# Kernel optimization log

Hardware: AMD Instinct MI355X
Metric: run time of the kernel (lower is better)

Reference implementation:

```python
import jax, jax.numpy as jnp
import numpy as np

MARGIN = 0.3
EPS = 1e-12


def setup_inputs() -> dict:
    key = jax.random.key(0)
    k1, k2, k3 = jax.random.split(key, 3)
    B, D = 8192, 1024
    features = jax.random.normal(k1, (B, D), dtype=jnp.float32)
    labels = jax.random.randint(k2, (B,), 0, 100, dtype=jnp.int64)
    domain_labels = jax.random.randint(k3, (B,), 0, 2, dtype=jnp.int64)
    return {"features": features, "labels": labels, "domain_labels": domain_labels}


def reference(features, labels, domain_labels):
    # L2-normalize rows (F.normalize: x / max(||x||, eps))
    norm = jnp.maximum(jnp.linalg.norm(features, axis=1, keepdims=True), EPS)
    f = features / norm

    herb = domain_labels == 0   # [B] anchors
    field = domain_labels == 1  # [B] candidates

    sq = jnp.sum(f * f, axis=1)                                   # [B]
    d2 = sq[:, None] + sq[None, :] - 2.0 * jnp.einsum('id,jd->ij', f, f)
    d = jnp.sqrt(jnp.maximum(d2, 0.0))                            # [B, B]

    same = labels[:, None] == labels[None, :]                     # [B, B]
    pair = herb[:, None] & field[None, :]
    pos_mask = pair & same
    neg_mask = pair & ~same

    INF = jnp.float32(jnp.inf)
    pos_min = jnp.min(jnp.where(pos_mask, d, INF), axis=1)        # [B]
    neg_min = jnp.min(jnp.where(neg_mask, d, INF), axis=1)        # [B]

    valid = herb & jnp.any(pos_mask, axis=1) & jnp.any(neg_mask, axis=1)
    # Substitute 0 for invalid rows BEFORE subtracting to avoid inf - inf.
    pos_s = jnp.where(valid, pos_min, 0.0)
    neg_s = jnp.where(valid, neg_min, 0.0)
    tl = jnp.maximum(pos_s - neg_s + MARGIN, 0.0)                 # [B]

    loss_sum = jnp.sum(jnp.where(valid, tl, 0.0))
    count = jnp.sum(valid.astype(jnp.float32))
    return jnp.where(count > 0, loss_sum / jnp.maximum(count, 1.0), 0.0)
```

## Files before the change

kernel.cpp:

```cpp
#include <hip/hip_runtime.h>


#define B_ROWS 8192
#define DIM    1024

typedef __bf16 bf16x8 __attribute__((ext_vector_type(8)));
typedef float  f32x4  __attribute__((ext_vector_type(4)));

__device__ __forceinline__ unsigned short f2bf_rne(float x) {
    unsigned u = __float_as_uint(x);
    unsigned r = (u + 0x7FFFu + ((u >> 16) & 1u)) >> 16;
    return (unsigned short)r;
}
__device__ __forceinline__ float bf2f(unsigned short h) {
    return __uint_as_float(((unsigned)h) << 16);
}

__device__ __forceinline__ void async_copy16(const void* g, void* l) {
    __builtin_amdgcn_global_load_lds(
        (const __attribute__((address_space(1))) unsigned int*)g,
        (__attribute__((address_space(3))) unsigned int*)l,
        16, 0, 0);
}

__global__ __launch_bounds__(256) void compute_slots(
    const int* __restrict__ dom, int* __restrict__ slotOf,
    unsigned* __restrict__ cnt)
{
    __shared__ int cnts[256];
    __shared__ int base[257];
    const int t = threadIdx.x;
    const int p0 = t * 32;

    unsigned mask = 0u; int c = 0;
    #pragma unroll
    for (int i = 0; i < 32; ++i) {
        const int isA = (dom[p0 + i] == 0) ? 1 : 0;
        mask |= ((unsigned)isA) << i;
        c += isA;
    }
    cnts[t] = c;
    __syncthreads();
    if (t == 0) {
        int acc = 0;
        for (int i = 0; i < 256; ++i) { base[i] = acc; acc += cnts[i]; }
        base[256] = acc;
        cnt[0] = (unsigned)acc;
    }
    __syncthreads();
    const int nA = base[256];
    int aB = base[t];
    #pragma unroll
    for (int i = 0; i < 32; ++i) {
        const int isA = (mask >> i) & 1;
        slotOf[p0 + i] = isA ? aB : nA + (p0 + i - aB);
        aB += isA;
    }
}

__global__ __launch_bounds__(256) void normalize_rows(
    const float* __restrict__ feat, const int* __restrict__ labels,
    const int* __restrict__ slotOf, unsigned short* __restrict__ G,
    int* __restrict__ labG, float* __restrict__ sqG)
{
    const int wv = threadIdx.x >> 6, lane = threadIdx.x & 63;
    const int row = blockIdx.x * 4 + wv;

    const float4* src = (const float4*)(feat + (size_t)row * DIM);
    float4 v[4];
    float ss = 0.0f;
    #pragma unroll
    for (int j = 0; j < 4; ++j) {
        v[j] = src[j * 64 + lane];
        ss += v[j].x * v[j].x + v[j].y * v[j].y + v[j].z * v[j].z + v[j].w * v[j].w;
    }
    #pragma unroll
    for (int s = 32; s > 0; s >>= 1) ss += __shfl_xor(ss, s);
    const float inv = 1.0f / fmaxf(sqrtf(ss), 1e-12f);

    const int slot = slotOf[row];
    unsigned short ub[16];
    float ss2 = 0.0f;
    #pragma unroll
    for (int j = 0; j < 4; ++j) {
        const float f0 = v[j].x * inv, f1 = v[j].y * inv,
                    f2 = v[j].z * inv, f3 = v[j].w * inv;
        ub[j * 4 + 0] = f2bf_rne(f0); ub[j * 4 + 1] = f2bf_rne(f1);
        ub[j * 4 + 2] = f2bf_rne(f2); ub[j * 4 + 3] = f2bf_rne(f3);
        #pragma unroll
        for (int q = 0; q < 4; ++q) {
            const float fr = bf2f(ub[j * 4 + q]);
            ss2 += fr * fr;
        }
    }
    #pragma unroll
    for (int s = 32; s > 0; s >>= 1) ss2 += __shfl_xor(ss2, s);
    if (lane == 0) {
        sqG[slot]  = ss2;
        labG[slot] = labels[row];
    }
    ushort4* dst = (ushort4*)(G + (size_t)slot * DIM);
    #pragma unroll
    for (int j = 0; j < 4; ++j) {
        ushort4 pk;
        pk.x = ub[j * 4 + 0]; pk.y = ub[j * 4 + 1];
        pk.z = ub[j * 4 + 2]; pk.w = ub[j * 4 + 3];
        dst[j * 64 + lane] = pk;
    }
}

__global__ __launch_bounds__(256) void tile_mindist(
    const unsigned short* __restrict__ G, const int* __restrict__ labG,
    const float* __restrict__ sqG, const unsigned* __restrict__ cnt,
    unsigned* __restrict__ posmin, unsigned* __restrict__ negmin)
{
    const int nA = (int)cnt[0];
    const int nF = B_ROWS - nA;
    const int nTA = (nA + 127) >> 7;
    const int nTF = (nF + 127) >> 7;
    const int total = nTA * nTF;

    __shared__ __align__(16) unsigned short S[2][2][128 * 32];

    const int t = threadIdx.x;
    const int lane = t & 63, w = t >> 6;
    const int wm = w >> 1, wn = w & 1;
    const int l15 = lane & 15, quad = lane >> 4;

    const int ch0 = 2 * w;
    const int crow = lane >> 2;
    const int cbyte = (lane & 3) * 16;

    const int rdA = (wm * 64 + l15) * 32 + quad * 8;
    const int rdF = (wn * 64 + l15) * 32 + quad * 8;

    const char* Gb = (const char*)G;

    for (int tile = blockIdx.x; tile < total; tile += gridDim.x) {
        const int tx = tile % nTA;
        const int ty = tile / nTA;
        const int rowA0 = tx * 128;
        const int rowF0 = nA + ty * 128;

        const char* ga[2]; const char* gf[2];
        #pragma unroll
        for (int h = 0; h < 2; ++h) {
            const int ch = ch0 + h;
            const int rA = rowA0 + 16 * ch + crow;
            int rF = rowF0 + 16 * ch + crow;
            if (rF > B_ROWS - 1) rF = B_ROWS - 1;
            ga[h] = Gb + (size_t)rA * (DIM * 2) + cbyte;
            gf[h] = Gb + (size_t)rF * (DIM * 2) + cbyte;
        }

        f32x4 acc[4][4] = {};

        #pragma unroll
        for (int h = 0; h < 2; ++h) {
            async_copy16(ga[h], &S[0][0][(ch0 + h) * 512]);
            async_copy16(gf[h], &S[0][1][(ch0 + h) * 512]);
        }
        __syncthreads();

        #pragma unroll 4
        for (int step = 0; step < 32; ++step) {
            const int cur = step & 1;
            const int nb = cur ^ 1;
            if (step < 31) {
                const int off = (step + 1) * 64;
                #pragma unroll
                for (int h = 0; h < 2; ++h) {
                    async_copy16(ga[h] + off, &S[nb][0][(ch0 + h) * 512]);
                    async_copy16(gf[h] + off, &S[nb][1][(ch0 + h) * 512]);
                }
            }

            const unsigned short* pa = &S[cur][0][rdA];
            const unsigned short* pf = &S[cur][1][rdF];
            bf16x8 a[4], b[4];
            #pragma unroll
            for (int fm = 0; fm < 4; ++fm) a[fm] = *(const bf16x8*)(pa + fm * 512);
            #pragma unroll
            for (int fn = 0; fn < 4; ++fn) b[fn] = *(const bf16x8*)(pf + fn * 512);
            #pragma unroll
            for (int fm = 0; fm < 4; ++fm)
                #pragma unroll
                for (int fn = 0; fn < 4; ++fn)
                    acc[fm][fn] = __builtin_amdgcn_mfma_f32_16x16x32_bf16(
                        a[fm], b[fn], acc[fm][fn], 0, 0, 0);

            __syncthreads();
        }

        const float INFV = __uint_as_float(0x7f800000u);
        float sqf[4]; int lf_[4]; bool vf[4];
        #pragma unroll
        for (int fn = 0; fn < 4; ++fn) {
            const int rf = rowF0 + wn * 64 + fn * 16 + l15;
            vf[fn] = rf < B_ROWS;
            const int rc = vf[fn] ? rf : (B_ROWS - 1);
            sqf[fn] = sqG[rc];
            lf_[fn] = labG[rc];
        }
        #pragma unroll
        for (int fm = 0; fm < 4; ++fm) {
            #pragma unroll
            for (int r = 0; r < 4; ++r) {
                const int ra = rowA0 + wm * 64 + fm * 16 + quad * 4 + r;
                const bool va = ra < nA;
                const int rac = va ? ra : 0;
                const float sqa = sqG[rac];
                const int la_ = labG[rac];
                float pmin = INFV, nmin = INFV;
                #pragma unroll
                for (int fn = 0; fn < 4; ++fn) {
                    const float dd = fmaxf(sqa + sqf[fn] - 2.0f * acc[fm][fn][r], 0.0f);
                    if (vf[fn]) {
                        if (la_ == lf_[fn]) pmin = fminf(pmin, dd);
                        else                nmin = fminf(nmin, dd);
                    }
                }
                #pragma unroll
                for (int s = 1; s < 16; s <<= 1) {
                    pmin = fminf(pmin, __shfl_xor(pmin, s));
                    nmin = fminf(nmin, __shfl_xor(nmin, s));
                }
                if (l15 == 0 && va) {
                    if (pmin < INFV) atomicMin(&posmin[ra], __float_as_uint(pmin));
                    if (nmin < INFV) atomicMin(&negmin[ra], __float_as_uint(nmin));
                }
            }
        }
        __syncthreads();
    }
}

__global__ __launch_bounds__(256) void reduce_loss(
    const unsigned* __restrict__ posmin, const unsigned* __restrict__ negmin,
    float* __restrict__ accum)
{
    const int i = blockIdx.x * 256 + threadIdx.x;
    const unsigned up = posmin[i], un = negmin[i];
    float tl = 0.0f, c = 0.0f;
    if (up != 0xFFFFFFFFu && un != 0xFFFFFFFFu) {
        const float pd = sqrtf(__uint_as_float(up));
        const float nd = sqrtf(__uint_as_float(un));
        tl = fmaxf(pd - nd + 0.3f, 0.0f);
        c = 1.0f;
    }
    #pragma unroll
    for (int s = 32; s > 0; s >>= 1) {
        tl += __shfl_down(tl, s);
        c  += __shfl_down(c, s);
    }
    __shared__ float sb[8];
    const int lane = threadIdx.x & 63, w = threadIdx.x >> 6;
    if (lane == 0) { sb[w] = tl; sb[4 + w] = c; }
    __syncthreads();
    if (threadIdx.x == 0) {
        atomicAdd(&accum[0], sb[0] + sb[1] + sb[2] + sb[3]);
        atomicAdd(&accum[1], sb[4] + sb[5] + sb[6] + sb[7]);
    }
}

__global__ void finalize(const float* __restrict__ accum, float* __restrict__ out) {
    const float s = accum[0], c = accum[1];
    out[0] = (c > 0.0f) ? s / fmaxf(c, 1.0f) : 0.0f;
}

extern "C" void kernel_launch(void* const* d_in, const int* in_sizes, int n_in,
                              void* d_out, int out_size, void* d_ws, size_t ws_size,
                              hipStream_t stream) {
    const float* feat  = (const float*)d_in[0];
    const int* labels  = (const int*)d_in[1];
    const int* dom     = (const int*)d_in[2];
    float* out = (float*)d_out;

    char* ws = (char*)d_ws;
    unsigned short* G   = (unsigned short*)(ws);
    int*      labG      = (int*)(ws + 16777216);
    float*    sqG       = (float*)(ws + 16809984);
    unsigned* posmin    = (unsigned*)(ws + 16842752);
    unsigned* negmin    = (unsigned*)(ws + 16875520);
    unsigned* cnt       = (unsigned*)(ws + 16908288);
    float*    accum     = (float*)(ws + 16908296);
    int*      slotOf    = (int*)(ws + 16842752);

    hipMemsetAsync(cnt, 0, 16, stream);

    compute_slots<<<1, 256, 0, stream>>>(dom, slotOf, cnt);
    normalize_rows<<<B_ROWS / 4, 256, 0, stream>>>(feat, labels, slotOf,
                                                   G, labG, sqG);

    hipMemsetAsync(posmin, 0xFF, 65536, stream);

    tile_mindist<<<1056, 256, 0, stream>>>(G, labG, sqG, cnt, posmin, negmin);

    reduce_loss<<<B_ROWS / 256, 256, 0, stream>>>(posmin, negmin, accum);
    finalize<<<1, 1, 0, stream>>>(accum, out);
}
```

Measured before the change: 180.5 us.

## Single-buffer K=64 LDS tiles in mindist GEMM and fuse loss reduction kernels

The tile GEMM's double-buffered 32-wide K slices are replaced by single-buffered 64-wide slices, so the main loop runs 16 steps with two MFMA K-substeps each. The idea is to halve loop iterations and barrier-paired steps. The cost is that the next slice's global loads now start only after compute finishes, so they no longer overlap the MFMAs. Separately, the multi-block reduce, its finalize kernel and the accumulator memset are replaced by one single-block kernel that writes the output directly. This removes launches and atomics but also drops the memset that zeroed the row counter.

After: 244.0 us. 1.35x slower.

```diff
diff --git a/kernel.cpp b/kernel.cpp
--- a/kernel.cpp
+++ b/kernel.cpp
@@ -120,19 +120,20 @@
     const int nTF = (nF + 127) >> 7;
     const int total = nTA * nTF;
 
-    __shared__ __align__(16) unsigned short S[2][2][128 * 32];
+    __shared__ __align__(16) unsigned short As[128 * 64];
+    __shared__ __align__(16) unsigned short Fs[128 * 64];
 
     const int t = threadIdx.x;
     const int lane = t & 63, w = t >> 6;
     const int wm = w >> 1, wn = w & 1;
     const int l15 = lane & 15, quad = lane >> 4;
 
-    const int ch0 = 2 * w;
-    const int crow = lane >> 2;
-    const int cbyte = (lane & 3) * 16;
-
-    const int rdA = (wm * 64 + l15) * 32 + quad * 8;
-    const int rdF = (wn * 64 + l15) * 32 + quad * 8;
+    const int c0 = 4 * w;
+    const int crow = lane >> 3;
+    const int cbyte = (lane & 7) * 16;
+
+    const int rdA = (wm * 64 + l15) * 64 + quad * 8;
+    const int rdF = (wn * 64 + l15) * 64 + quad * 8;
 
     const char* Gb = (const char*)G;
 
@@ -142,12 +143,12 @@
         const int rowA0 = tx * 128;
         const int rowF0 = nA + ty * 128;
 
-        const char* ga[2]; const char* gf[2];
-        #pragma unroll
-        for (int h = 0; h < 2; ++h) {
-            const int ch = ch0 + h;
-            const int rA = rowA0 + 16 * ch + crow;
-            int rF = rowF0 + 16 * ch + crow;
+        const char* ga[4]; const char* gf[4];
+        #pragma unroll
+        for (int h = 0; h < 4; ++h) {
+            const int c = c0 + h;
+            const int rA = rowA0 + 8 * c + crow;
+            int rF = rowF0 + 8 * c + crow;
             if (rF > B_ROWS - 1) rF = B_ROWS - 1;
             ga[h] = Gb + (size_t)rA * (DIM * 2) + cbyte;
             gf[h] = Gb + (size_t)rF * (DIM * 2) + cbyte;
@@ -156,40 +157,42 @@
         f32x4 acc[4][4] = {};
 
         #pragma unroll
-        for (int h = 0; h < 2; ++h) {
-            async_copy16(ga[h], &S[0][0][(ch0 + h) * 512]);
-            async_copy16(gf[h], &S[0][1][(ch0 + h) * 512]);
-        }
-        __syncthreads();
-
-        #pragma unroll 4
-        for (int step = 0; step < 32; ++step) {
-            const int cur = step & 1;
-            const int nb = cur ^ 1;
-            if (step < 31) {
-                const int off = (step + 1) * 64;
-                #pragma unroll
-                for (int h = 0; h < 2; ++h) {
-                    async_copy16(ga[h] + off, &S[nb][0][(ch0 + h) * 512]);
-                    async_copy16(gf[h] + off, &S[nb][1][(ch0 + h) * 512]);
+        for (int h = 0; h < 4; ++h) {
+            async_copy16(ga[h], &As[(c0 + h) * 512]);
+            async_copy16(gf[h], &Fs[(c0 + h) * 512]);
+        }
+
+        for (int step = 0; step < 16; ++step) {
+            __syncthreads();
+
+            bf16x8 a[4][2], b[4][2];
+            #pragma unroll
+            for (int u = 0; u < 2; ++u) {
+                #pragma unroll
+                for (int fm = 0; fm < 4; ++fm)
+                    a[fm][u] = *(const bf16x8*)(&As[rdA + fm * 1024 + u * 32]);
+                #pragma unroll
+                for (int fn = 0; fn < 4; ++fn)
+                    b[fn][u] = *(const bf16x8*)(&Fs[rdF + fn * 1024 + u * 32]);
+            }
+            #pragma unroll
+            for (int u = 0; u < 2; ++u)
+                #pragma unroll
+                for (int fm = 0; fm < 4; ++fm)
+                    #pragma unroll
+                    for (int fn = 0; fn < 4; ++fn)
+                        acc[fm][fn] = __builtin_amdgcn_mfma_f32_16x16x32_bf16(
+                            a[fm][u], b[fn][u], acc[fm][fn], 0, 0, 0);
+
+            __syncthreads();
+            if (step < 15) {
+                const int off = (step + 1) * 128;
+                #pragma unroll
+                for (int h = 0; h < 4; ++h) {
+                    async_copy16(ga[h] + off, &As[(c0 + h) * 512]);
+                    async_copy16(gf[h] + off, &Fs[(c0 + h) * 512]);
                 }
             }
-
-            const unsigned short* pa = &S[cur][0][rdA];
-            const unsigned short* pf = &S[cur][1][rdF];
-            bf16x8 a[4], b[4];
-            #pragma unroll
-            for (int fm = 0; fm < 4; ++fm) a[fm] = *(const bf16x8*)(pa + fm * 512);
-            #pragma unroll
-            for (int fn = 0; fn < 4; ++fn) b[fn] = *(const bf16x8*)(pf + fn * 512);
-            #pragma unroll
-            for (int fm = 0; fm < 4; ++fm)
-                #pragma unroll
-                for (int fn = 0; fn < 4; ++fn)
-                    acc[fm][fn] = __builtin_amdgcn_mfma_f32_16x16x32_bf16(
-                        a[fm], b[fn], acc[fm][fn], 0, 0, 0);
-
-            __syncthreads();
         }
 
         const float INFV = __uint_as_float(0x7f800000u);
@@ -235,18 +238,23 @@
     }
 }
 
-__global__ __launch_bounds__(256) void reduce_loss(
+__global__ __launch_bounds__(256) void reduce_one(
     const unsigned* __restrict__ posmin, const unsigned* __restrict__ negmin,
-    float* __restrict__ accum)
+    float* __restrict__ out)
 {
-    const int i = blockIdx.x * 256 + threadIdx.x;
-    const unsigned up = posmin[i], un = negmin[i];
+    const int t = threadIdx.x;
+    const int lane = t & 63, w = t >> 6;
     float tl = 0.0f, c = 0.0f;
-    if (up != 0xFFFFFFFFu && un != 0xFFFFFFFFu) {
-        const float pd = sqrtf(__uint_as_float(up));
-        const float nd = sqrtf(__uint_as_float(un));
-        tl = fmaxf(pd - nd + 0.3f, 0.0f);
-        c = 1.0f;
+    #pragma unroll
+    for (int j = 0; j < 32; ++j) {
+        const int i = j * 256 + t;
+        const unsigned up = posmin[i], un = negmin[i];
+        if (up != 0xFFFFFFFFu && un != 0xFFFFFFFFu) {
+            const float pd = sqrtf(__uint_as_float(up));
+            const float nd = sqrtf(__uint_as_float(un));
+            tl += fmaxf(pd - nd + 0.3f, 0.0f);
+            c += 1.0f;
+        }
     }
     #pragma unroll
     for (int s = 32; s > 0; s >>= 1) {
@@ -254,18 +262,13 @@
         c  += __shfl_down(c, s);
     }
     __shared__ float sb[8];
-    const int lane = threadIdx.x & 63, w = threadIdx.x >> 6;
     if (lane == 0) { sb[w] = tl; sb[4 + w] = c; }
     __syncthreads();
-    if (threadIdx.x == 0) {
-        atomicAdd(&accum[0], sb[0] + sb[1] + sb[2] + sb[3]);
-        atomicAdd(&accum[1], sb[4] + sb[5] + sb[6] + sb[7]);
-    }
-}
-
-__global__ void finalize(const float* __restrict__ accum, float* __restrict__ out) {
-    const float s = accum[0], c = accum[1];
-    out[0] = (c > 0.0f) ? s / fmaxf(c, 1.0f) : 0.0f;
+    if (t == 0) {
+        const float s = sb[0] + sb[1] + sb[2] + sb[3];
+        const float cc = sb[4] + sb[5] + sb[6] + sb[7];
+        out[0] = (cc > 0.0f) ? s / fmaxf(cc, 1.0f) : 0.0f;
+    }
 }
 
 extern "C" void kernel_launch(void* const* d_in, const int* in_sizes, int n_in,
@@ -283,10 +286,7 @@
     unsigned* posmin    = (unsigned*)(ws + 16842752);
     unsigned* negmin    = (unsigned*)(ws + 16875520);
     unsigned* cnt       = (unsigned*)(ws + 16908288);
-    float*    accum     = (float*)(ws + 16908296);
     int*      slotOf    = (int*)(ws + 16842752);
-
-    hipMemsetAsync(cnt, 0, 16, stream);
 
     compute_slots<<<1, 256, 0, stream>>>(dom, slotOf, cnt);
     normalize_rows<<<B_ROWS / 4, 256, 0, stream>>>(feat, labels, slotOf,
@@ -296,6 +296,5 @@
 
     tile_mindist<<<1056, 256, 0, stream>>>(G, labG, sqG, cnt, posmin, negmin);
 
-    reduce_loss<<<B_ROWS / 256, 256, 0, stream>>>(posmin, negmin, accum);
-    finalize<<<1, 1, 0, stream>>>(accum, out);
-}
+    reduce_one<<<1, 256, 0, stream>>>(posmin, negmin, out);
+}
```

## Map tile strips to XCDs for L2 reuse and fuse loss reduction kernels

Applied to the files above, without the earlier changes.

Tiles are now assigned so that the blocks landing on each XCD (blockIdx & 7) share a contiguous strip of candidate tiles, which keeps those candidate rows resident in that XCD's L2 instead of spreading tiles across all caches. The separate reduce and finalize kernels, the accumulator and one memset are replaced by a single-block kernel that reduces all 8192 rows and writes the output directly. This removes launch and atomic overhead. In exchange the final reduction runs on one block only, and correctness now relies on compute_slots initialising cnt without the removed memset.

New measurement: 182.9 us. Within noise of the previous version (+1.3%).

```diff
diff --git a/kernel.cpp b/kernel.cpp
--- a/kernel.cpp
+++ b/kernel.cpp
@@ -118,7 +118,13 @@
     const int nF = B_ROWS - nA;
     const int nTA = (nA + 127) >> 7;
     const int nTF = (nF + 127) >> 7;
-    const int total = nTA * nTF;
+    if (nTA == 0 || nTF == 0) return;
+
+    const int strip = (nTF + 7) >> 3;
+    const int xcd  = blockIdx.x & 7;
+    const int slot = blockIdx.x >> 3;
+    const int tyBase = xcd * strip;
+    const int nloc = nTA * strip;
 
     __shared__ __align__(16) unsigned short S[2][2][128 * 32];
 
@@ -136,9 +142,10 @@
 
     const char* Gb = (const char*)G;
 
-    for (int tile = blockIdx.x; tile < total; tile += gridDim.x) {
-        const int tx = tile % nTA;
-        const int ty = tile / nTA;
+    for (int idx = slot; idx < nloc; idx += 132) {
+        const int ty = tyBase + idx / nTA;
+        if (ty >= nTF) break;
+        const int tx = idx % nTA;
         const int rowA0 = tx * 128;
         const int rowF0 = nA + ty * 128;
 
@@ -235,18 +242,23 @@
     }
 }
 
-__global__ __launch_bounds__(256) void reduce_loss(
+__global__ __launch_bounds__(256) void reduce_one(
     const unsigned* __restrict__ posmin, const unsigned* __restrict__ negmin,
-    float* __restrict__ accum)
+    float* __restrict__ out)
 {
-    const int i = blockIdx.x * 256 + threadIdx.x;
-    const unsigned up = posmin[i], un = negmin[i];
+    const int t = threadIdx.x;
+    const int lane = t & 63, w = t >> 6;
     float tl = 0.0f, c = 0.0f;
-    if (up != 0xFFFFFFFFu && un != 0xFFFFFFFFu) {
-        const float pd = sqrtf(__uint_as_float(up));
-        const float nd = sqrtf(__uint_as_float(un));
-        tl = fmaxf(pd - nd + 0.3f, 0.0f);
-        c = 1.0f;
+    #pragma unroll
+    for (int j = 0; j < 32; ++j) {
+        const int i = j * 256 + t;
+        const unsigned up = posmin[i], un = negmin[i];
+        if (up != 0xFFFFFFFFu && un != 0xFFFFFFFFu) {
+            const float pd = sqrtf(__uint_as_float(up));
+            const float nd = sqrtf(__uint_as_float(un));
+            tl += fmaxf(pd - nd + 0.3f, 0.0f);
+            c += 1.0f;
+        }
     }
     #pragma unroll
     for (int s = 32; s > 0; s >>= 1) {
@@ -254,18 +266,13 @@
         c  += __shfl_down(c, s);
     }
     __shared__ float sb[8];
-    const int lane = threadIdx.x & 63, w = threadIdx.x >> 6;
     if (lane == 0) { sb[w] = tl; sb[4 + w] = c; }
     __syncthreads();
-    if (threadIdx.x == 0) {
-        atomicAdd(&accum[0], sb[0] + sb[1] + sb[2] + sb[3]);
-        atomicAdd(&accum[1], sb[4] + sb[5] + sb[6] + sb[7]);
-    }
-}
-
-__global__ void finalize(const float* __restrict__ accum, float* __restrict__ out) {
-    const float s = accum[0], c = accum[1];
-    out[0] = (c > 0.0f) ? s / fmaxf(c, 1.0f) : 0.0f;
+    if (t == 0) {
+        const float s = sb[0] + sb[1] + sb[2] + sb[3];
+        const float cc = sb[4] + sb[5] + sb[6] + sb[7];
+        out[0] = (cc > 0.0f) ? s / fmaxf(cc, 1.0f) : 0.0f;
+    }
 }
 
 extern "C" void kernel_launch(void* const* d_in, const int* in_sizes, int n_in,
@@ -283,10 +290,7 @@
     unsigned* posmin    = (unsigned*)(ws + 16842752);
     unsigned* negmin    = (unsigned*)(ws + 16875520);
     unsigned* cnt       = (unsigned*)(ws + 16908288);
-    float*    accum     = (float*)(ws + 16908296);
     int*      slotOf    = (int*)(ws + 16842752);
-
-    hipMemsetAsync(cnt, 0, 16, stream);
 
     compute_slots<<<1, 256, 0, stream>>>(dom, slotOf, cnt);
     normalize_rows<<<B_ROWS / 4, 256, 0, stream>>>(feat, labels, slotOf,
@@ -296,6 +300,5 @@
 
     tile_mindist<<<1056, 256, 0, stream>>>(G, labG, sqG, cnt, posmin, negmin);
 
-    reduce_loss<<<B_ROWS / 256, 256, 0, stream>>>(posmin, negmin, accum);
-    finalize<<<1, 1, 0, stream>>>(accum, out);
-}
+    reduce_one<<<1, 256, 0, stream>>>(posmin, negmin, out);
+}
```
